# Performance work log

Measured on AMD Instinct MI355X. Metric: run time of the kernel, lower is better.

The kernel has to match this reference:

```python
import jax, jax.numpy as jnp
import numpy as np

BIG = 1e9  # finite 'null' sentinel standing in for +inf (min / shortest-path DP)


def _minplus_scan(a, c):
    """Solve v[j] = min(c[j], v[j-1] + a[j]) along last axis (v[0] = c[0] when a[0]=BIG).
    Min-plus linear recurrence -> associative scan over pairs (a, c)."""
    def combine(x, y):
        a1, c1 = x
        a2, c2 = y
        return a1 + a2, jnp.minimum(c2, c1 + a2)
    _, v = jax.lax.associative_scan(combine, (a, c), axis=-1)
    return v


def setup_inputs() -> dict:
    key = jax.random.key(0)
    images = jax.random.uniform(key, (2048, 64, 64), dtype=jnp.float32)
    return {"images": images}


def reference(images):
    # Grid DAG on HxW nodes; edges (i,j-1)->(i,j), (i-1,j)->(i,j), (i-1,j-1)->(i,j).
    # GraphLayer: edge potential theta(u->v) = (img[u] + img[v]) / 2.
    # SPFunction: shortest-path DP from (0,0) to (H-1,W-1); returns path length per sample.
    B, H, W = images.shape
    img = images
    t_right = 0.5 * (img[:, :, :-1] + img[:, :, 1:])      # [B, H,   W-1]
    t_down  = 0.5 * (img[:, :-1, :] + img[:, 1:, :])      # [B, H-1, W  ]
    t_diag  = 0.5 * (img[:, :-1, :-1] + img[:, 1:, 1:])   # [B, H-1, W-1]

    # Row 0: only right edges -> plain cumulative sum.
    d0 = jnp.concatenate(
        [jnp.zeros((B, 1), dtype=img.dtype), jnp.cumsum(t_right[:, 0, :], axis=-1)],
        axis=-1,
    )  # [B, W]

    a_pad = jnp.full((B, 1), jnp.float32(BIG), dtype=img.dtype)

    def row_step(prev, xs):
        td, tdg, tr = xs  # td: [B,W], tdg: [B,W-1], tr: [B,W-1]
        c = prev + td                                  # candidate via down edge
        diag_cand = prev[:, :-1] + tdg                 # candidate via diag edge
        c = c.at[:, 1:].set(jnp.minimum(c[:, 1:], diag_cand))
        a = jnp.concatenate([a_pad, tr], axis=-1)      # right-edge weights, a[0]=BIG
        v = _minplus_scan(a, c)                        # fold in right edges within the row
        return v, None

    xs = (
        jnp.moveaxis(t_down, 1, 0),            # [H-1, B, W]
        jnp.moveaxis(t_diag, 1, 0),            # [H-1, B, W-1]
        jnp.moveaxis(t_right[:, 1:, :], 1, 0), # [H-1, B, W-1]
    )
    d_last, _ = jax.lax.scan(row_step, d0, xs)
    return d_last[:, -1]  # [B] shortest-path lengths
```

## Files before the change

### kernel.cpp

```cpp
#include <hip/hip_runtime.h>

#define BIG 1e9f

#define RD(W) \
    "v_add_u32 %[ik], 1, %[ik]\n\t" \
    "v_med3_i32 %[ic], %[ik], 0, 63\n\t" \
    "v_lshl_add_u32 %[ad], %[ic], 8, %[sb]\n\t" \
    "ds_read_b32 " W ", %[ad]\n\t"

#define CMP(W, XN, XO) \
    "s_waitcnt lgkmcnt(12)\n\t" \
    "v_mov_b32 " XN ", %[vbig]\n\t" \
    "v_mov_b32_dpp " XN ", %[e] wave_shr:1 row_mask:0xf bank_mask:0xf\n\t" \
    "v_min3_f32 %[tp], " XN ", %[e], " XO "\n\t" \
    "v_add_f32 %[e], %[tp], " W "\n\t"

#define SLOT(WISS, WCON, XN, XO) RD(WISS) CMP(WCON, XN, XO)

__global__ __launch_bounds__(128) void dp_diag_kernel(const float* __restrict__ img,
                                                      float* __restrict__ out, int B) {
    __shared__ __align__(16) float smem[2][4096];
    const int lane = threadIdx.x & 63;
    const int wave = threadIdx.x >> 6;
    const int b = (blockIdx.x << 1) + wave;
    if (b >= B) return;

    float* s = smem[wave];
    {
        const float4* g4 = (const float4*)(img + ((size_t)b << 12));
        float4* s4 = (float4*)s;
        #pragma unroll
        for (int t = 0; t < 16; ++t)
            s4[(t << 6) + lane] = g4[(t << 6) + lane];
    }

    float e  = (lane == 0) ? 0.5f * s[0] : BIG;
    float x0 = BIG, x1 = BIG;
    float w0 = 0, w1 = 0, w2 = 0, w3 = 0, w4 = 0, w5 = 0, w6 = 0,
          w7 = 0, w8 = 0, w9 = 0, w10 = 0, w11 = 0, w12 = 0, w13 = 0;
    int ik = -lane;
    int ic = 0; unsigned ad = 0; float tp = 0;
    const float    vbig  = BIG;
    const unsigned sbase = (unsigned)(uintptr_t)s + ((unsigned)lane << 2);

    asm volatile(
        RD("%[w1]") RD("%[w2]") RD("%[w3]") RD("%[w4]") RD("%[w5]") RD("%[w6]")
        RD("%[w7]") RD("%[w8]") RD("%[w9]") RD("%[w10]") RD("%[w11]") RD("%[w12]")
        "s_nop 2\n\t"
        : [ik]"+v"(ik), [ic]"+v"(ic), [ad]"+v"(ad),
          [w1]"+v"(w1), [w2]"+v"(w2), [w3]"+v"(w3), [w4]"+v"(w4),
          [w5]"+v"(w5), [w6]"+v"(w6), [w7]"+v"(w7), [w8]"+v"(w8),
          [w9]"+v"(w9), [w10]"+v"(w10), [w11]"+v"(w11), [w12]"+v"(w12)
        : [sb]"v"(sbase)
        : "memory");

    #pragma unroll 1
    for (int it = 0; it < 9; ++it) {
        asm volatile(
            SLOT("%[w13]", "%[w1]",  "%[x0]", "%[x1]")
            SLOT("%[w0]",  "%[w2]",  "%[x1]", "%[x0]")
            SLOT("%[w1]",  "%[w3]",  "%[x0]", "%[x1]")
            SLOT("%[w2]",  "%[w4]",  "%[x1]", "%[x0]")
            SLOT("%[w3]",  "%[w5]",  "%[x0]", "%[x1]")
            SLOT("%[w4]",  "%[w6]",  "%[x1]", "%[x0]")
            SLOT("%[w5]",  "%[w7]",  "%[x0]", "%[x1]")
            SLOT("%[w6]",  "%[w8]",  "%[x1]", "%[x0]")
            SLOT("%[w7]",  "%[w9]",  "%[x0]", "%[x1]")
            SLOT("%[w8]",  "%[w10]", "%[x1]", "%[x0]")
            SLOT("%[w9]",  "%[w11]", "%[x0]", "%[x1]")
            SLOT("%[w10]", "%[w12]", "%[x1]", "%[x0]")
            SLOT("%[w11]", "%[w13]", "%[x0]", "%[x1]")
            SLOT("%[w12]", "%[w0]",  "%[x1]", "%[x0]")
            : [e]"+v"(e), [x0]"+v"(x0), [x1]"+v"(x1), [tp]"+v"(tp),
              [ik]"+v"(ik), [ic]"+v"(ic), [ad]"+v"(ad),
              [w0]"+v"(w0), [w1]"+v"(w1), [w2]"+v"(w2), [w3]"+v"(w3),
              [w4]"+v"(w4), [w5]"+v"(w5), [w6]"+v"(w6), [w7]"+v"(w7),
              [w8]"+v"(w8), [w9]"+v"(w9), [w10]"+v"(w10), [w11]"+v"(w11),
              [w12]"+v"(w12), [w13]"+v"(w13)
            : [sb]"v"(sbase), [vbig]"v"(vbig)
            : "memory");
    }
    asm volatile("s_waitcnt lgkmcnt(0)\n\t" ::: "memory");

    if (lane == 63) out[b] = e - 0.5f * s[4095];
}

extern "C" void kernel_launch(void* const* d_in, const int* in_sizes, int n_in,
                              void* d_out, int out_size, void* d_ws, size_t ws_size,
                              hipStream_t stream) {
    const float* img = (const float*)d_in[0];
    float* out = (float*)d_out;
    const int B = out_size;
    const int threads = 128;
    const int grid = (B + 1) / 2;
    dp_diag_kernel<<<grid, threads, 0, stream>>>(img, out, B);
}
```

Before: 73.50 us.

## Stream image into LDS via global_load_lds and overlap with anti-diagonal DP

Replaces the register-staged global-to-LDS copy with direct global_load_lds transfers. Instead of waiting for the whole image before starting, it places partial vmcnt waits between the first four unrolled DP bodies, so the wavefront sweep can begin once the early rows arrive. This targets the load latency at the start of each wave. The risk is that the vmcnt thresholds must match the order in which rows are consumed, and the LDS writes from the async loads may need extra sync to be visible.

```diff
diff --git a/kernel.cpp b/kernel.cpp
--- a/kernel.cpp
+++ b/kernel.cpp
@@ -17,6 +17,31 @@
 
 #define SLOT(WISS, WCON, XN, XO) RD(WISS) CMP(WCON, XN, XO)
 
+#define BODY14 \
+    asm volatile( \
+        SLOT("%[w13]", "%[w1]",  "%[x0]", "%[x1]") \
+        SLOT("%[w0]",  "%[w2]",  "%[x1]", "%[x0]") \
+        SLOT("%[w1]",  "%[w3]",  "%[x0]", "%[x1]") \
+        SLOT("%[w2]",  "%[w4]",  "%[x1]", "%[x0]") \
+        SLOT("%[w3]",  "%[w5]",  "%[x0]", "%[x1]") \
+        SLOT("%[w4]",  "%[w6]",  "%[x1]", "%[x0]") \
+        SLOT("%[w5]",  "%[w7]",  "%[x0]", "%[x1]") \
+        SLOT("%[w6]",  "%[w8]",  "%[x1]", "%[x0]") \
+        SLOT("%[w7]",  "%[w9]",  "%[x0]", "%[x1]") \
+        SLOT("%[w8]",  "%[w10]", "%[x1]", "%[x0]") \
+        SLOT("%[w9]",  "%[w11]", "%[x0]", "%[x1]") \
+        SLOT("%[w10]", "%[w12]", "%[x1]", "%[x0]") \
+        SLOT("%[w11]", "%[w13]", "%[x0]", "%[x1]") \
+        SLOT("%[w12]", "%[w0]",  "%[x1]", "%[x0]") \
+        : [e]"+v"(e), [x0]"+v"(x0), [x1]"+v"(x1), [tp]"+v"(tp), \
+          [ik]"+v"(ik), [ic]"+v"(ic), [ad]"+v"(ad), \
+          [w0]"+v"(w0), [w1]"+v"(w1), [w2]"+v"(w2), [w3]"+v"(w3), \
+          [w4]"+v"(w4), [w5]"+v"(w5), [w6]"+v"(w6), [w7]"+v"(w7), \
+          [w8]"+v"(w8), [w9]"+v"(w9), [w10]"+v"(w10), [w11]"+v"(w11), \
+          [w12]"+v"(w12), [w13]"+v"(w13) \
+        : [sb]"v"(sbase), [vbig]"v"(vbig) \
+        : "memory")
+
 __global__ __launch_bounds__(128) void dp_diag_kernel(const float* __restrict__ img,
                                                       float* __restrict__ out, int B) {
     __shared__ __align__(16) float smem[2][4096];
@@ -27,12 +52,15 @@
 
     float* s = smem[wave];
     {
-        const float4* g4 = (const float4*)(img + ((size_t)b << 12));
-        float4* s4 = (float4*)s;
+        const float* g = img + ((size_t)b << 12) + (lane << 2);
         #pragma unroll
         for (int t = 0; t < 16; ++t)
-            s4[(t << 6) + lane] = g4[(t << 6) + lane];
+            __builtin_amdgcn_global_load_lds(
+                (const __attribute__((address_space(1))) void*)(g + (t << 8)),
+                (__attribute__((address_space(3))) void*)(s + (t << 8)),
+                16, 0, 0);
     }
+    asm volatile("s_waitcnt vmcnt(12)\n\t" ::: "memory");
 
     float e  = (lane == 0) ? 0.5f * s[0] : BIG;
     float x0 = BIG, x1 = BIG;
@@ -54,32 +82,17 @@
         : [sb]"v"(sbase)
         : "memory");
 
+    asm volatile("s_waitcnt vmcnt(9)\n\t" ::: "memory");
+    BODY14;
+    asm volatile("s_waitcnt vmcnt(5)\n\t" ::: "memory");
+    BODY14;
+    asm volatile("s_waitcnt vmcnt(2)\n\t" ::: "memory");
+    BODY14;
+    asm volatile("s_waitcnt vmcnt(0)\n\t" ::: "memory");
+    BODY14;
     #pragma unroll 1
-    for (int it = 0; it < 9; ++it) {
-        asm volatile(
-            SLOT("%[w13]", "%[w1]",  "%[x0]", "%[x1]")
-            SLOT("%[w0]",  "%[w2]",  "%[x1]", "%[x0]")
-            SLOT("%[w1]",  "%[w3]",  "%[x0]", "%[x1]")
-            SLOT("%[w2]",  "%[w4]",  "%[x1]", "%[x0]")
-            SLOT("%[w3]",  "%[w5]",  "%[x0]", "%[x1]")
-            SLOT("%[w4]",  "%[w6]",  "%[x1]", "%[x0]")
-            SLOT("%[w5]",  "%[w7]",  "%[x0]", "%[x1]")
-            SLOT("%[w6]",  "%[w8]",  "%[x1]", "%[x0]")
-            SLOT("%[w7]",  "%[w9]",  "%[x0]", "%[x1]")
-            SLOT("%[w8]",  "%[w10]", "%[x1]", "%[x0]")
-            SLOT("%[w9]",  "%[w11]", "%[x0]", "%[x1]")
-            SLOT("%[w10]", "%[w12]", "%[x1]", "%[x0]")
-            SLOT("%[w11]", "%[w13]", "%[x0]", "%[x1]")
-            SLOT("%[w12]", "%[w0]",  "%[x1]", "%[x0]")
-            : [e]"+v"(e), [x0]"+v"(x0), [x1]"+v"(x1), [tp]"+v"(tp),
-              [ik]"+v"(ik), [ic]"+v"(ic), [ad]"+v"(ad),
-              [w0]"+v"(w0), [w1]"+v"(w1), [w2]"+v"(w2), [w3]"+v"(w3),
-              [w4]"+v"(w4), [w5]"+v"(w5), [w6]"+v"(w6), [w7]"+v"(w7),
-              [w8]"+v"(w8), [w9]"+v"(w9), [w10]"+v"(w10), [w11]"+v"(w11),
-              [w12]"+v"(w12), [w13]"+v"(w13)
-            : [sb]"v"(sbase), [vbig]"v"(vbig)
-            : "memory");
-    }
+    for (int it = 0; it < 5; ++it)
+        BODY14;
     asm volatile("s_waitcnt lgkmcnt(0)\n\t" ::: "memory");
 
     if (lane == 63) out[b] = e - 0.5f * s[4095];
```

Result: faster. 71.64 us (-2.5%).
